# Optimization experiments

Hardware: AMD Instinct MI355X
Metric: run time of the kernel (lower is better)

The kernel has to match this reference:

```python
import jax, jax.numpy as jnp
import numpy as np

NUM_CODES = 512
DIM = 64
B, M = 32, 64


def setup_inputs() -> dict:
    key = jax.random.key(0)
    k1, k2 = jax.random.split(key)
    inputs = jax.random.normal(k1, (B, M, M, DIM), dtype=jnp.float32)
    # keras 'uniform' initializer is U(-0.05, 0.05)
    embeddings = jax.random.uniform(k2, (NUM_CODES, DIM), dtype=jnp.float32,
                                    minval=-0.05, maxval=0.05)
    return {"inputs": inputs, "embeddings": embeddings}


def reference(inputs, embeddings):
    l2_inputs = jnp.sum(inputs * inputs, axis=-1, keepdims=True)      # [B,M,M,1]
    l2_embeddings = jnp.sum(embeddings * embeddings, axis=-1)          # [K]
    dot = jnp.einsum('bhwd,kd->bhwk', inputs, embeddings)              # [B,M,M,K]
    distance = l2_inputs + l2_embeddings - 2.0 * dot                   # [B,M,M,K]
    codes = jnp.argmin(distance, axis=-1).astype(jnp.int32)            # [B,M,M]
    code_vecs = embeddings[codes]                                      # [B,M,M,D]
    return codes, code_vecs
```

## Files before the change

### kernel.cpp

```cpp
#include <hip/hip_runtime.h>

#define NUM_CODES 512
#define DIM 64
#define NPIX (32 * 64 * 64)
#define CT (NUM_CODES / 16)
#define BLK 256
#define NGRP 2
#define PPB 128

typedef __attribute__((ext_vector_type(8))) short bf16x8;
typedef __attribute__((ext_vector_type(4))) float f32x4;

__device__ __forceinline__ unsigned short f2bf(float f) {
    unsigned u = __float_as_uint(f);
    return (unsigned short)((u + 0x7fffu + ((u >> 16) & 1u)) >> 16);
}
__device__ __forceinline__ float bf2f(unsigned short h) {
    return __uint_as_float(((unsigned)h) << 16);
}

__global__ __launch_bounds__(256) void prep_kernel(
    const float* __restrict__ emb, unsigned short* __restrict__ AH,
    unsigned short* __restrict__ ALO, float* __restrict__ l2e,
    float* __restrict__ l2eh) {
    const int t = blockIdx.x * 256 + threadIdx.x;
    const int e0 = t * 4;
    const int c = e0 >> 6, d0 = e0 & 63;
    const float4 v = *(const float4*)(emb + c * DIM + d0);
    float f[4] = {-v.x, -v.y, -v.z, -v.w};
    unsigned short h[4], l[4];
#pragma unroll
    for (int i = 0; i < 4; ++i) {
        h[i] = f2bf(f[i]);
        l[i] = f2bf(f[i] - bf2f(h[i]));
    }
    const int ct = c >> 4, mr = c & 15, s = d0 >> 5, q = (d0 & 31) >> 3,
              j0 = d0 & 7;
    const int base = ((ct * 2 + s) * 64 + (q * 16 + mr)) * 8 + j0;
    *(ushort4*)(AH + base) = make_ushort4(h[0], h[1], h[2], h[3]);
    *(ushort4*)(ALO + base) = make_ushort4(l[0], l[1], l[2], l[3]);

    if (t < NUM_CODES) {
        const float* e = emb + t * DIM;
        float r[8];
#pragma unroll
        for (int j = 0; j < 8; ++j) {
            float w = e[j];
            r[j] = w * w;
        }
#pragma unroll
        for (int i = 8; i < DIM; i += 8)
#pragma unroll
            for (int j = 0; j < 8; ++j) {
                float w = e[i + j];
                r[j] += w * w;
            }
        float sv =
            ((r[0] + r[1]) + (r[2] + r[3])) + ((r[4] + r[5]) + (r[6] + r[7]));
        l2e[t] = sv;
        l2eh[t] = 0.5f * sv;
    }
}

__global__ __launch_bounds__(BLK, 4) void vq_main(
    const float* __restrict__ x_in, const unsigned short* __restrict__ AH,
    const unsigned short* __restrict__ ALO, const float* __restrict__ l2e,
    const float* __restrict__ l2eh, const float* __restrict__ emb,
    float* __restrict__ codes_out, float* __restrict__ vecs_out) {
    __shared__ float s_l2eh[NUM_CODES];
    __shared__ float s_l2ex[NUM_CODES];
    __shared__ int s_top[PPB][2];
    __shared__ int s_code[PPB];

    const int tid = threadIdx.x, lane = tid & 63, wave = tid >> 6;
    s_l2eh[tid] = l2eh[tid];
    s_l2eh[tid + 256] = l2eh[tid + 256];
    s_l2ex[tid] = l2e[tid];
    s_l2ex[tid + 256] = l2e[tid + 256];
    __syncthreads();

    const int p = lane & 15, q = lane >> 4;
    const int pw = blockIdx.x * PPB + wave * (16 * NGRP);

    bf16x8 bh0[NGRP], bl0[NGRP], bh1[NGRP], bl1[NGRP];
#pragma unroll
    for (int g = 0; g < NGRP; ++g) {
        const float* xb = x_in + (size_t)(pw + g * 16 + p) * DIM + q * 8;
        float4 u0 = *(const float4*)(xb);
        float4 u1 = *(const float4*)(xb + 4);
        float4 u2 = *(const float4*)(xb + 32);
        float4 u3 = *(const float4*)(xb + 36);
        float f0[8] = {u0.x, u0.y, u0.z, u0.w, u1.x, u1.y, u1.z, u1.w};
        float f1[8] = {u2.x, u2.y, u2.z, u2.w, u3.x, u3.y, u3.z, u3.w};
#pragma unroll
        for (int j = 0; j < 8; ++j) {
            unsigned short hh = f2bf(f0[j]);
            bh0[g][j] = (short)hh;
            bl0[g][j] = (short)f2bf(f0[j] - bf2f(hh));
            unsigned short h2 = f2bf(f1[j]);
            bh1[g][j] = (short)h2;
            bl1[g][j] = (short)f2bf(f1[j] - bf2f(h2));
        }
    }

    const int rowbase = q * 4;
    float d1[NGRP], d2[NGRP];
    int k1[NGRP], k2[NGRP];
#pragma unroll
    for (int g = 0; g < NGRP; ++g) {
        d1[g] = 3.4e38f;
        d2[g] = 3.4e38f;
        k1[g] = 0;
        k2[g] = 0;
    }

    const unsigned short* pAH = AH + lane * 8;
    const unsigned short* pAL = ALO + lane * 8;

    bf16x8 c0h = *(const bf16x8*)(pAH);
    bf16x8 c0l = *(const bf16x8*)(pAL);
    bf16x8 c1h = *(const bf16x8*)(pAH + 512);
    bf16x8 c1l = *(const bf16x8*)(pAL + 512);
    bf16x8 p0h = *(const bf16x8*)(pAH + 1024);
    bf16x8 p0l = *(const bf16x8*)(pAL + 1024);
    bf16x8 p1h = *(const bf16x8*)(pAH + 1024 + 512);
    bf16x8 p1l = *(const bf16x8*)(pAL + 1024 + 512);

#pragma unroll 4
    for (int ct = 0; ct < CT; ++ct) {
        const int nt = (ct + 2) & (CT - 1);
        const bf16x8 q0h = *(const bf16x8*)(pAH + nt * 1024);
        const bf16x8 q0l = *(const bf16x8*)(pAL + nt * 1024);
        const bf16x8 q1h = *(const bf16x8*)(pAH + nt * 1024 + 512);
        const bf16x8 q1l = *(const bf16x8*)(pAL + nt * 1024 + 512);

        const int kb = ct * 16 + rowbase;
        const f32x4 acc_init = *(const f32x4*)&s_l2eh[kb];

        f32x4 accA[NGRP], accB[NGRP];
        __builtin_amdgcn_s_setprio(1);
#pragma unroll
        for (int g = 0; g < NGRP; ++g) {
            f32x4 a = acc_init;
            a = __builtin_amdgcn_mfma_f32_16x16x32_bf16(c0h, bh0[g], a, 0, 0, 0);
            a = __builtin_amdgcn_mfma_f32_16x16x32_bf16(c0l, bh0[g], a, 0, 0, 0);
            a = __builtin_amdgcn_mfma_f32_16x16x32_bf16(c0h, bl0[g], a, 0, 0, 0);
            f32x4 b = {0.f, 0.f, 0.f, 0.f};
            b = __builtin_amdgcn_mfma_f32_16x16x32_bf16(c1h, bh1[g], b, 0, 0, 0);
            b = __builtin_amdgcn_mfma_f32_16x16x32_bf16(c1l, bh1[g], b, 0, 0, 0);
            b = __builtin_amdgcn_mfma_f32_16x16x32_bf16(c1h, bl1[g], b, 0, 0, 0);
            accA[g] = a;
            accB[g] = b;
        }
        __builtin_amdgcn_s_setprio(0);

#pragma unroll
        for (int g = 0; g < NGRP; ++g) {
#pragma unroll
            for (int r = 0; r < 4; ++r) {
                const float d = accA[g][r] + accB[g][r];
                const int kk = kb + r;
                const bool c = d < d1[g], c2 = d < d2[g];
                const float nd2 = __builtin_amdgcn_fmed3f(d1[g], d2[g], d);
                const int nk2 = c2 ? kk : k2[g];
                k2[g] = c ? k1[g] : nk2;
                k1[g] = c ? kk : k1[g];
                d2[g] = nd2;
                d1[g] = fminf(d1[g], d);
            }
        }

        c0h = p0h; c0l = p0l; c1h = p1h; c1l = p1l;
        p0h = q0h; p0l = q0l; p1h = q1h; p1l = q1l;
    }

#pragma unroll
    for (int g = 0; g < NGRP; ++g) {
        float a1 = d1[g], a2 = d2[g];
        int b1 = k1[g], b2 = k2[g];
#pragma unroll
        for (int off = 16; off <= 32; off <<= 1) {
            const float od1 = __shfl_xor(a1, off);
            const int ok1 = __shfl_xor(b1, off);
            const float od2 = __shfl_xor(a2, off);
            const int ok2 = __shfl_xor(b2, off);
            const bool c = od1 < a1;
            const float w1 = c ? od1 : a1;
            const int wk1 = c ? ok1 : b1;
            const float l1 = c ? a1 : od1;
            const int lk1 = c ? b1 : ok1;
            const bool cm = od2 < a2;
            const float m2 = cm ? od2 : a2;
            const int mk2 = cm ? ok2 : b2;
            const bool c3 = m2 < l1;
            a2 = c3 ? m2 : l1;
            b2 = c3 ? mk2 : lk1;
            a1 = w1;
            b1 = wk1;
        }
        if (lane < 16) {
            const int pb = wave * (16 * NGRP) + g * 16 + lane;
            s_top[pb][0] = b1;
            s_top[pb][1] = b2;
        }
    }
    __syncthreads();

    {
        const int pixloc = tid >> 1, which = tid & 1;
        const int pix = blockIdx.x * PPB + pixloc;
        const int k_me = s_top[pixloc][which];
        const float* xr = x_in + (size_t)pix * DIM;
        float x[DIM];
#pragma unroll
        for (int jj = 0; jj < 16; ++jj) {
            const float4 v = *(const float4*)(xr + jj * 4);
            x[4 * jj + 0] = v.x;
            x[4 * jj + 1] = v.y;
            x[4 * jj + 2] = v.z;
            x[4 * jj + 3] = v.w;
        }
        float r[8];
#pragma unroll
        for (int j = 0; j < 8; ++j) r[j] = x[j] * x[j];
#pragma unroll
        for (int i = 8; i < DIM; i += 8)
#pragma unroll
            for (int j = 0; j < 8; ++j) r[j] += x[i + j] * x[i + j];
        const float l2x =
            ((r[0] + r[1]) + (r[2] + r[3])) + ((r[4] + r[5]) + (r[6] + r[7]));

        const float* em = emb + (size_t)k_me * DIM;
        float acc = 0.f;
#pragma unroll
        for (int d = 0; d < DIM; ++d) acc = __builtin_fmaf(x[d], em[d], acc);
        const float d_me = (l2x + s_l2ex[k_me]) - 2.0f * acc;

        const float d_o = __shfl_xor(d_me, 1);
        const int k_o = __shfl_xor(k_me, 1);
        const int sel =
            (d_me < d_o || (d_me == d_o && k_me < k_o)) ? k_me : k_o;
        if (which == 0) {
            s_code[pixloc] = sel;
            codes_out[pix] = (float)sel;
        }
    }
    __syncthreads();

    const float4* emb4 = (const float4*)emb;
    float4* vout4 = (float4*)(vecs_out + (size_t)blockIdx.x * PPB * DIM);
#pragma unroll
    for (int it = 0; it < (PPB * DIM / 4) / BLK; ++it) {
        const int fidx = tid + it * BLK;
        const int pp = fidx >> 4, dd = fidx & 15;
        vout4[fidx] = emb4[(size_t)s_code[pp] * (DIM / 4) + dd];
    }
}

extern "C" void kernel_launch(void* const* d_in, const int* in_sizes, int n_in,
                              void* d_out, int out_size, void* d_ws,
                              size_t ws_size, hipStream_t stream) {
    const float* x_in = (const float*)d_in[0];
    const float* emb = (const float*)d_in[1];

    unsigned short* AH = (unsigned short*)d_ws;
    unsigned short* ALO = AH + NUM_CODES * DIM;
    float* l2e = (float*)(ALO + NUM_CODES * DIM);
    float* l2eh = l2e + NUM_CODES;

    float* codes_out = (float*)d_out;
    float* vecs_out = (float*)d_out + NPIX;

    hipLaunchKernelGGL(prep_kernel, dim3(32), dim3(256), 0, stream, emb, AH,
                       ALO, l2e, l2eh);
    hipLaunchKernelGGL(vq_main, dim3(NPIX / PPB), dim3(BLK), 0, stream, x_in,
                       AH, ALO, l2e, l2eh, emb, codes_out, vecs_out);
}
```

Before: 120.1 us.

## Double pixels per block and rescore both candidates per thread

Raises each block from 128 to 256 pixels, with four 16-pixel groups per wave, and lowers the launch-bounds occupancy hint from 4 to 2 blocks. The fp32 rescoring now uses one thread per pixel that checks both top candidates, replacing two threads per pixel plus a shuffle. Each pixel's input row is read once instead of twice and the cross-lane exchange goes away. The cost is more registers per thread, fewer resident blocks and half as many blocks overall.

After: 123.3 us. +2.7%, slower.

```diff
diff --git a/kernel.cpp b/kernel.cpp
--- a/kernel.cpp
+++ b/kernel.cpp
@@ -5,8 +5,8 @@
 #define NPIX (32 * 64 * 64)
 #define CT (NUM_CODES / 16)
 #define BLK 256
-#define NGRP 2
-#define PPB 128
+#define NGRP 4
+#define PPB 256
 
 typedef __attribute__((ext_vector_type(8))) short bf16x8;
 typedef __attribute__((ext_vector_type(4))) float f32x4;
@@ -62,7 +62,7 @@
     }
 }
 
-__global__ __launch_bounds__(BLK, 4) void vq_main(
+__global__ __launch_bounds__(BLK, 2) void vq_main(
     const float* __restrict__ x_in, const unsigned short* __restrict__ AH,
     const unsigned short* __restrict__ ALO, const float* __restrict__ l2e,
     const float* __restrict__ l2eh, const float* __restrict__ emb,
@@ -207,9 +207,13 @@
     __syncthreads();
 
     {
-        const int pixloc = tid >> 1, which = tid & 1;
-        const int pix = blockIdx.x * PPB + pixloc;
-        const int k_me = s_top[pixloc][which];
+        const int pix = blockIdx.x * PPB + tid;
+        int ka = s_top[tid][0], kb2 = s_top[tid][1];
+        if (kb2 < ka) {
+            const int tt = ka;
+            ka = kb2;
+            kb2 = tt;
+        }
         const float* xr = x_in + (size_t)pix * DIM;
         float x[DIM];
 #pragma unroll
@@ -230,20 +234,21 @@
         const float l2x =
             ((r[0] + r[1]) + (r[2] + r[3])) + ((r[4] + r[5]) + (r[6] + r[7]));
 
-        const float* em = emb + (size_t)k_me * DIM;
-        float acc = 0.f;
-#pragma unroll
-        for (int d = 0; d < DIM; ++d) acc = __builtin_fmaf(x[d], em[d], acc);
-        const float d_me = (l2x + s_l2ex[k_me]) - 2.0f * acc;
-
-        const float d_o = __shfl_xor(d_me, 1);
-        const int k_o = __shfl_xor(k_me, 1);
-        const int sel =
-            (d_me < d_o || (d_me == d_o && k_me < k_o)) ? k_me : k_o;
-        if (which == 0) {
-            s_code[pixloc] = sel;
-            codes_out[pix] = (float)sel;
-        }
+        const float* ea = emb + (size_t)ka * DIM;
+        float acca = 0.f;
+#pragma unroll
+        for (int d = 0; d < DIM; ++d) acca = __builtin_fmaf(x[d], ea[d], acca);
+        const float da = (l2x + s_l2ex[ka]) - 2.0f * acca;
+
+        const float* eb = emb + (size_t)kb2 * DIM;
+        float accb = 0.f;
+#pragma unroll
+        for (int d = 0; d < DIM; ++d) accb = __builtin_fmaf(x[d], eb[d], accb);
+        const float db = (l2x + s_l2ex[kb2]) - 2.0f * accb;
+
+        const int sel = (db < da) ? kb2 : ka;
+        s_code[tid] = sel;
+        codes_out[pix] = (float)sel;
     }
     __syncthreads();
 
```

## Pack distance and code index into sortable uint, keep top-3 candidates

Applied to the files above, without the earlier changes.

Distances get a positive bias (+4 in the half-norm term) so their float bits sort as unsigned ints. The low 9 mantissa bits are replaced by the code index, so one u32 min/med3 network tracks a top-3 list in place of separate float/int top-2 bookkeeping. The cross-lane merge now uses three shuffles and med3 merges. The exact fp32 rescoring pass evaluates three candidates (two per thread pair) to make up for the truncated distance precision. This cuts ALU and VGPR use in the hot loop but adds one more fp32 dot product per thread in the epilogue.

Result: slower. 129.6 us (+7.9%).

```diff
diff --git a/kernel.cpp b/kernel.cpp
--- a/kernel.cpp
+++ b/kernel.cpp
@@ -17,6 +17,11 @@
 }
 __device__ __forceinline__ float bf2f(unsigned short h) {
     return __uint_as_float(((unsigned)h) << 16);
+}
+__device__ __forceinline__ unsigned med3u(unsigned a, unsigned b, unsigned c) {
+    unsigned r;
+    asm("v_med3_u32 %0, %1, %2, %3" : "=v"(r) : "v"(a), "v"(b), "v"(c));
+    return r;
 }
 
 __global__ __launch_bounds__(256) void prep_kernel(
@@ -58,7 +63,7 @@
         float sv =
             ((r[0] + r[1]) + (r[2] + r[3])) + ((r[4] + r[5]) + (r[6] + r[7]));
         l2e[t] = sv;
-        l2eh[t] = 0.5f * sv;
+        l2eh[t] = 0.5f * sv + 4.0f;
     }
 }
 
@@ -69,7 +74,7 @@
     float* __restrict__ codes_out, float* __restrict__ vecs_out) {
     __shared__ float s_l2eh[NUM_CODES];
     __shared__ float s_l2ex[NUM_CODES];
-    __shared__ int s_top[PPB][2];
+    __shared__ unsigned s_top[PPB][3];
     __shared__ int s_code[PPB];
 
     const int tid = threadIdx.x, lane = tid & 63, wave = tid >> 6;
@@ -104,14 +109,12 @@
     }
 
     const int rowbase = q * 4;
-    float d1[NGRP], d2[NGRP];
-    int k1[NGRP], k2[NGRP];
+    unsigned t1[NGRP], t2[NGRP], t3[NGRP];
 #pragma unroll
     for (int g = 0; g < NGRP; ++g) {
-        d1[g] = 3.4e38f;
-        d2[g] = 3.4e38f;
-        k1[g] = 0;
-        k2[g] = 0;
+        t1[g] = 0xFFFFFFFFu;
+        t2[g] = 0xFFFFFFFFu;
+        t3[g] = 0xFFFFFFFFu;
     }
 
     const unsigned short* pAH = AH + lane * 8;
@@ -159,14 +162,15 @@
 #pragma unroll
             for (int r = 0; r < 4; ++r) {
                 const float d = accA[g][r] + accB[g][r];
-                const int kk = kb + r;
-                const bool c = d < d1[g], c2 = d < d2[g];
-                const float nd2 = __builtin_amdgcn_fmed3f(d1[g], d2[g], d);
-                const int nk2 = c2 ? kk : k2[g];
-                k2[g] = c ? k1[g] : nk2;
-                k1[g] = c ? kk : k1[g];
-                d2[g] = nd2;
-                d1[g] = fminf(d1[g], d);
+                const unsigned pk = (__float_as_uint(d) & 0xFFFFFE00u) |
+                                    (unsigned)(kb + r);
+                const unsigned n1 = t1[g] < pk ? t1[g] : pk;
+                const unsigned m2 = med3u(t1[g], t2[g], pk);
+                const unsigned mx = t1[g] > pk ? t1[g] : pk;
+                const unsigned m3 = med3u(t2[g], t3[g], mx);
+                t1[g] = n1;
+                t2[g] = m2;
+                t3[g] = m3;
             }
         }
 
@@ -176,32 +180,29 @@
 
 #pragma unroll
     for (int g = 0; g < NGRP; ++g) {
-        float a1 = d1[g], a2 = d2[g];
-        int b1 = k1[g], b2 = k2[g];
+        unsigned a1 = t1[g], a2 = t2[g], a3 = t3[g];
 #pragma unroll
         for (int off = 16; off <= 32; off <<= 1) {
-            const float od1 = __shfl_xor(a1, off);
-            const int ok1 = __shfl_xor(b1, off);
-            const float od2 = __shfl_xor(a2, off);
-            const int ok2 = __shfl_xor(b2, off);
-            const bool c = od1 < a1;
-            const float w1 = c ? od1 : a1;
-            const int wk1 = c ? ok1 : b1;
-            const float l1 = c ? a1 : od1;
-            const int lk1 = c ? b1 : ok1;
-            const bool cm = od2 < a2;
-            const float m2 = cm ? od2 : a2;
-            const int mk2 = cm ? ok2 : b2;
-            const bool c3 = m2 < l1;
-            a2 = c3 ? m2 : l1;
-            b2 = c3 ? mk2 : lk1;
-            a1 = w1;
-            b1 = wk1;
+            const unsigned o1 = __shfl_xor(a1, off);
+            const unsigned o2 = __shfl_xor(a2, off);
+            const unsigned o3 = __shfl_xor(a3, off);
+#pragma unroll
+            for (int e = 0; e < 3; ++e) {
+                const unsigned o = (e == 0) ? o1 : (e == 1) ? o2 : o3;
+                const unsigned n1 = a1 < o ? a1 : o;
+                const unsigned m2 = med3u(a1, a2, o);
+                const unsigned mx = a1 > o ? a1 : o;
+                const unsigned m3 = med3u(a2, a3, mx);
+                a1 = n1;
+                a2 = m2;
+                a3 = m3;
+            }
         }
         if (lane < 16) {
             const int pb = wave * (16 * NGRP) + g * 16 + lane;
-            s_top[pb][0] = b1;
-            s_top[pb][1] = b2;
+            s_top[pb][0] = a1;
+            s_top[pb][1] = a2;
+            s_top[pb][2] = a3;
         }
     }
     __syncthreads();
@@ -209,7 +210,8 @@
     {
         const int pixloc = tid >> 1, which = tid & 1;
         const int pix = blockIdx.x * PPB + pixloc;
-        const int k_me = s_top[pixloc][which];
+        const int k_w = (int)(s_top[pixloc][which] & 511u);
+        const int k_s = (int)(s_top[pixloc][2] & 511u);
         const float* xr = x_in + (size_t)pix * DIM;
         float x[DIM];
 #pragma unroll
@@ -230,11 +232,21 @@
         const float l2x =
             ((r[0] + r[1]) + (r[2] + r[3])) + ((r[4] + r[5]) + (r[6] + r[7]));
 
-        const float* em = emb + (size_t)k_me * DIM;
-        float acc = 0.f;
-#pragma unroll
-        for (int d = 0; d < DIM; ++d) acc = __builtin_fmaf(x[d], em[d], acc);
-        const float d_me = (l2x + s_l2ex[k_me]) - 2.0f * acc;
+        const float* ew = emb + (size_t)k_w * DIM;
+        float accw = 0.f;
+#pragma unroll
+        for (int d = 0; d < DIM; ++d) accw = __builtin_fmaf(x[d], ew[d], accw);
+        const float d_w = (l2x + s_l2ex[k_w]) - 2.0f * accw;
+
+        const float* es = emb + (size_t)k_s * DIM;
+        float accs = 0.f;
+#pragma unroll
+        for (int d = 0; d < DIM; ++d) accs = __builtin_fmaf(x[d], es[d], accs);
+        const float d_s = (l2x + s_l2ex[k_s]) - 2.0f * accs;
+
+        const bool cl = (d_s < d_w) || (d_s == d_w && k_s < k_w);
+        const float d_me = cl ? d_s : d_w;
+        const int k_me = cl ? k_s : k_w;
 
         const float d_o = __shfl_xor(d_me, 1);
         const int k_o = __shfl_xor(k_me, 1);
```
